# Performance work log

Measured on AMD Instinct MI355X. Metric: run time of the kernel, lower is better.

The kernel has to match this reference:

```python
import jax, jax.numpy as jnp
import numpy as np

N, T, DIN, DH = 100000, 512, 256, 256


def setup_inputs() -> dict:
    key = jax.random.key(0)
    ks = jax.random.split(key, 7)
    s_in = 1.0 / np.sqrt(DH)  # torch GRU init scale
    X = jax.random.normal(ks[0], (N, DIN), dtype=jnp.float32)
    H = (jax.random.uniform(ks[1], (N, T)) < 0.02).astype(jnp.float32)
    W_ih = jax.random.uniform(ks[2], (3 * DH, DIN), minval=-s_in, maxval=s_in, dtype=jnp.float32)
    W_hh = jax.random.uniform(ks[3], (3 * DH, DH), minval=-s_in, maxval=s_in, dtype=jnp.float32)
    b_ih = jax.random.uniform(ks[4], (3 * DH,), minval=-s_in, maxval=s_in, dtype=jnp.float32)
    b_hh = jax.random.uniform(ks[5], (3 * DH,), minval=-s_in, maxval=s_in, dtype=jnp.float32)
    w_att = jax.random.uniform(ks[6], (DH,), minval=-s_in, maxval=s_in, dtype=jnp.float32)
    return {"X": X, "H": H, "W_ih": W_ih, "W_hh": W_hh, "b_ih": b_ih, "b_hh": b_hh, "w_att": w_att}


def _gru(visit_emb, W_ih, W_hh, b_ih, b_hh):
    # torch GRU gate order: r, z, n
    dh = W_hh.shape[1]
    gx = visit_emb @ W_ih.T + b_ih  # [T, 3H] precomputed input projections

    def step(h, gx_t):
        gh = h @ W_hh.T + b_hh  # [3H]
        r = jax.nn.sigmoid(gx_t[:dh] + gh[:dh])
        z = jax.nn.sigmoid(gx_t[dh:2 * dh] + gh[dh:2 * dh])
        n = jnp.tanh(gx_t[2 * dh:] + r * gh[2 * dh:])
        h_new = (1.0 - z) * n + z * h
        return h_new, h_new

    h0 = jnp.zeros((dh,), dtype=visit_emb.dtype)
    _, hs = jax.lax.scan(step, h0, gx)
    return hs  # [T, H]


def reference(X, H, W_ih, W_hh, b_ih, b_hh, w_att):
    visit_emb = H.T @ X  # [T, Din] incidence aggregation
    hidden = _gru(visit_emb, W_ih, W_hh, b_ih, b_hh)  # [T, H]
    alpha = jax.nn.softmax(hidden @ w_att, axis=0)  # [T]
    # diag(alpha) @ hidden summed over T == alpha-weighted sum
    return jnp.einsum("t,th->h", alpha, hidden)
```

## Files before the change

kernel.cpp:

```cpp
#include <hip/hip_runtime.h>
#include <hip/hip_bf16.h>

#define N_ROWS 100000
#define T_DIM  512
#define DIN    256
#define DH     256
#define KC     800
#define NSTEP  25
#define NCHUNK 125

typedef __attribute__((ext_vector_type(8))) short s16x8;
typedef __attribute__((ext_vector_type(4))) float f32x4;
typedef _Float16 h2 __attribute__((ext_vector_type(2)));
typedef _Float16 h8 __attribute__((ext_vector_type(8)));

#if __has_builtin(__builtin_amdgcn_fdot2)
static __device__ __forceinline__ float dot2f(h2 a, h2 b, float c) {
  return __builtin_amdgcn_fdot2(a, b, c, false);
}
#else
static __device__ __forceinline__ float dot2f(h2 a, h2 b, float c) {
  return c + (float)a[0] * (float)b[0] + (float)a[1] * (float)b[1];
}
#endif

static __device__ __forceinline__ unsigned bf16pair(float lo, float hi) {
  unsigned a = __builtin_bit_cast(unsigned, lo);
  unsigned b = __builtin_bit_cast(unsigned, hi);
  a = (a + 0x7fffu + ((a >> 16) & 1u)) >> 16;
  b = (b + 0x7fffu + ((b >> 16) & 1u)) & 0xffff0000u;
  return a | b;
}

__global__ __launch_bounds__(512, 2) void k_agg_mfma(
    const float* __restrict__ X, const float* __restrict__ Hm,
    float* __restrict__ ve, float* __restrict__ ve_part, int use_part)
{
  __shared__ unsigned smem[8192];
  const int tid  = threadIdx.x;
  const int mt   = blockIdx.x & 1;
  const int kc   = blockIdx.x >> 1;
  const int m0   = mt * 256;
  const int k0   = kc * KC;
  const int lane = tid & 63;
  const int wv   = tid >> 6;
  const int wm   = wv >> 2, wn = wv & 3;

  f32x4 acc[8][4] = {};

  const int kp0 = tid >> 6;
  const int kp1 = kp0 + 8;
  const int gg  = tid & 63;

  float4 ra0, ra1, ra2, ra3, rb0, rb1, rb2, rb3;

  auto load_tile = [&](int kt) {
    const size_t kb = (size_t)(k0 + kt * 32);
    const float* pa0 = &Hm[(kb + 2 * kp0) * T_DIM + m0 + gg * 4];
    ra0 = *(const float4*)pa0;
    ra1 = *(const float4*)(pa0 + T_DIM);
    const float* pa1 = &Hm[(kb + 2 * kp1) * T_DIM + m0 + gg * 4];
    ra2 = *(const float4*)pa1;
    ra3 = *(const float4*)(pa1 + T_DIM);
    const float* pb0 = &X[(kb + 2 * kp0) * DIN + gg * 4];
    rb0 = *(const float4*)pb0;
    rb1 = *(const float4*)(pb0 + DIN);
    const float* pb1 = &X[(kb + 2 * kp1) * DIN + gg * 4];
    rb2 = *(const float4*)pb1;
    rb3 = *(const float4*)(pb1 + DIN);
  };

  auto store_tile = [&]() {
#pragma unroll
    for (int d = 0; d < 4; ++d) {
      const int m  = gg * 4 + d;
      const int sw = d << 2;
      smem[m * 16 + (kp0 ^ sw)]        = bf16pair(((const float*)&ra0)[d], ((const float*)&ra1)[d]);
      smem[m * 16 + (kp1 ^ sw)]        = bf16pair(((const float*)&ra2)[d], ((const float*)&ra3)[d]);
      smem[4096 + m * 16 + (kp0 ^ sw)] = bf16pair(((const float*)&rb0)[d], ((const float*)&rb1)[d]);
      smem[4096 + m * 16 + (kp1 ^ sw)] = bf16pair(((const float*)&rb2)[d], ((const float*)&rb3)[d]);
    }
  };

  auto compute = [&]() {
    const uint4* sv = (const uint4*)smem;
    s16x8 af[8], bfr[4];
#pragma unroll
    for (int fm = 0; fm < 8; ++fm) {
      const int m = wm * 128 + fm * 16 + (lane & 15);
      af[fm] = __builtin_bit_cast(s16x8, sv[m * 4 + ((lane >> 4) ^ (m & 3))]);
    }
#pragma unroll
    for (int fn = 0; fn < 4; ++fn) {
      const int n = wn * 64 + fn * 16 + (lane & 15);
      bfr[fn] = __builtin_bit_cast(s16x8, sv[1024 + n * 4 + ((lane >> 4) ^ (n & 3))]);
    }
#pragma unroll
    for (int fm = 0; fm < 8; ++fm)
#pragma unroll
      for (int fn = 0; fn < 4; ++fn)
        acc[fm][fn] = __builtin_amdgcn_mfma_f32_16x16x32_bf16(af[fm], bfr[fn], acc[fm][fn], 0, 0, 0);
  };

  load_tile(0);
  store_tile();
  for (int kt = 0; kt < NSTEP; ++kt) {
    __syncthreads();
    if (kt + 1 < NSTEP) load_tile(kt + 1);
    compute();
    __syncthreads();
    if (kt + 1 < NSTEP) store_tile();
  }

  if (use_part) {
    float* dst = ve_part + (size_t)kc * (512 * 256);
#pragma unroll
    for (int fm = 0; fm < 8; ++fm) {
      const int r0 = m0 + wm * 128 + fm * 16 + (lane >> 4) * 4;
#pragma unroll
      for (int fn = 0; fn < 4; ++fn) {
        const int cc = wn * 64 + fn * 16 + (lane & 15);
#pragma unroll
        for (int q = 0; q < 4; ++q)
          dst[(size_t)(r0 + q) * 256 + cc] = acc[fm][fn][q];
      }
    }
  } else {
#pragma unroll
    for (int fm = 0; fm < 8; ++fm) {
      const int r0 = m0 + wm * 128 + fm * 16 + (lane >> 4) * 4;
#pragma unroll
      for (int fn = 0; fn < 4; ++fn) {
        const int cc = wn * 64 + fn * 16 + (lane & 15);
#pragma unroll
        for (int q = 0; q < 4; ++q)
          atomicAdd(&ve[(size_t)(r0 + q) * 256 + cc], acc[fm][fn][q]);
      }
    }
  }
}

__global__ __launch_bounds__(256) void k_gx(
    const float* __restrict__ vesrc, int npart,
    const float* __restrict__ Wih, const float* __restrict__ bih,
    float* __restrict__ gx)
{
  __shared__ float vl[DIN];
  const int t = blockIdx.x, j = threadIdx.x;
  float s = 0.f;
  for (int p = 0; p < npart; ++p) s += vesrc[(size_t)p * (512 * 256) + t * DIN + j];
  vl[j] = s;
  __syncthreads();
  float a0 = bih[j], a1 = bih[256 + j], a2 = bih[512 + j];
  const float* __restrict__ w0 = &Wih[(size_t)j * DIN];
  const float* __restrict__ w1 = &Wih[(size_t)(j + 256) * DIN];
  const float* __restrict__ w2 = &Wih[(size_t)(j + 512) * DIN];
#pragma unroll 4
  for (int k = 0; k < DIN; ++k) {
    const float v = vl[k];
    a0 = fmaf(w0[k], v, a0);
    a1 = fmaf(w1[k], v, a1);
    a2 = fmaf(w2[k], v, a2);
  }
  gx[t * 768 + j]       = a0;
  gx[t * 768 + 256 + j] = a1;
  gx[t * 768 + 512 + j] = a2;
}

__global__ __launch_bounds__(768, 3) void k_gru_att(
    const float* __restrict__ Whh, const float* __restrict__ bhh,
    const float* __restrict__ gx, const float* __restrict__ watt,
    float* __restrict__ hs, float* __restrict__ out)
{
  __shared__ h8 hbuf8[DH / 8];
  __shared__ float gh[768];
  __shared__ float red[2];
  const int j = threadIdx.x;

  h2 w[128];
  {
    const float2* __restrict__ row = (const float2*)&Whh[(size_t)j * DH];
#pragma unroll
    for (int c = 0; c < 128; ++c) {
      const float2 p = row[c];
      h2 v; v[0] = (_Float16)p.x; v[1] = (_Float16)p.y;
      w[c] = v;
    }
  }
  float bhr = 0.f, bhz = 0.f, bhn = 0.f, h = 0.f;
  if (j < 256) { bhr = bhh[j]; bhz = bhh[256 + j]; bhn = bhh[512 + j]; }
  _Float16* hb = (_Float16*)hbuf8;
  if (j < 256) hb[j] = (_Float16)0.f;
  __syncthreads();

  for (int t = 0; t < T_DIM; ++t) {
    float gxr = 0.f, gxz = 0.f, gxn = 0.f;
    if (j < 256) {
      gxr = gx[t * 768 + j];
      gxz = gx[t * 768 + 256 + j];
      gxn = gx[t * 768 + 512 + j];
    }
    float a0 = 0.f, a1 = 0.f, a2 = 0.f, a3 = 0.f;
#pragma unroll
    for (int c = 0; c < 32; ++c) {
      const h8 hv = hbuf8[c];
      const h2 p0 = __builtin_shufflevector(hv, hv, 0, 1);
      const h2 p1 = __builtin_shufflevector(hv, hv, 2, 3);
      const h2 p2 = __builtin_shufflevector(hv, hv, 4, 5);
      const h2 p3 = __builtin_shufflevector(hv, hv, 6, 7);
      a0 = dot2f(w[4 * c + 0], p0, a0);
      a1 = dot2f(w[4 * c + 1], p1, a1);
      a2 = dot2f(w[4 * c + 2], p2, a2);
      a3 = dot2f(w[4 * c + 3], p3, a3);
    }
    gh[j] = (a0 + a1) + (a2 + a3);
    __syncthreads();
    if (j < 256) {
      const float pr = gxr + gh[j] + bhr;
      const float pz = gxz + gh[256 + j] + bhz;
      const float gn = gh[512 + j] + bhn;
      const float r = 1.f / (1.f + __expf(-pr));
      const float z = 1.f / (1.f + __expf(-pz));
      const float pn = gxn + r * gn;
      const float n = 2.f / (1.f + __expf(-2.f * pn)) - 1.f;
      h = (1.f - z) * n + z * h;
      hs[t * DH + j] = h;
      hb[j] = (_Float16)h;
    }
    __syncthreads();
  }

  if (j < T_DIM) {
    const float* __restrict__ hr = &hs[j * DH];
    float s = 0.f;
#pragma unroll 4
    for (int k = 0; k < DH; ++k) s = fmaf(hr[k], watt[k], s);
    gh[j] = s;
  }
  __syncthreads();
  if (j < 64) {
    float m = -1e30f;
#pragma unroll
    for (int i = 0; i < 8; ++i) m = fmaxf(m, gh[j * 8 + i]);
#pragma unroll
    for (int off = 32; off > 0; off >>= 1) m = fmaxf(m, __shfl_down(m, off));
    if (j == 0) red[0] = m;
  }
  __syncthreads();
  const float M = red[0];
  if (j < T_DIM) gh[j] = __expf(gh[j] - M);
  __syncthreads();
  if (j < 64) {
    float s = 0.f;
#pragma unroll
    for (int i = 0; i < 8; ++i) s += gh[j * 8 + i];
#pragma unroll
    for (int off = 32; off > 0; off >>= 1) s += __shfl_down(s, off);
    if (j == 0) red[1] = s;
  }
  __syncthreads();
  const float inv = 1.f / red[1];
  if (j < 256) {
    float acc = 0.f;
    for (int t = 0; t < T_DIM; ++t) acc = fmaf(gh[t], hs[t * DH + j], acc);
    out[j] = acc * inv;
  }
}

extern "C" void kernel_launch(void* const* d_in, const int* in_sizes, int n_in,
                              void* d_out, int out_size, void* d_ws, size_t ws_size,
                              hipStream_t stream) {
  const float* X    = (const float*)d_in[0];
  const float* H    = (const float*)d_in[1];
  const float* Wih  = (const float*)d_in[2];
  const float* Whh  = (const float*)d_in[3];
  const float* bih  = (const float*)d_in[4];
  const float* bhh  = (const float*)d_in[5];
  const float* watt = (const float*)d_in[6];
  float* out = (float*)d_out;

  char* ws = (char*)d_ws;
  float* gx      = (float*)ws;
  float* hs      = (float*)(ws + 1572864);
  float* ve      = (float*)(ws + 2097152);
  float* ve_part = (float*)(ws + 2621440);

  const size_t need_part = 2621440 + 65536000;
  const int use_part = (ws_size >= need_part) ? 1 : 0;

  if (!use_part)
    hipMemsetAsync(ve, 0, T_DIM * DIN * sizeof(float), stream);

  k_agg_mfma<<<2 * NCHUNK, 512, 0, stream>>>(X, H, ve, ve_part, use_part);
  k_gx<<<T_DIM, 256, 0, stream>>>(use_part ? ve_part : ve, use_part ? NCHUNK : 1,
                                  Wih, bih, gx);
  k_gru_att<<<1, 768, 0, stream>>>(Whh, bhh, gx, watt, hs, out);
}
```

Before: 972.3 us.

## Give each GRU thread all three gate rows to drop shared-memory exchange

Shrinks the recurrent GRU kernel from 768 to 256 threads, with each thread holding its r, z and n weight rows in registers (384 half2 values). Each thread now computes all three gate dot products itself, so the gh shared-memory round trip and one barrier phase per step are gone, and every thread does gate math instead of a third of them sitting idle. In exchange each thread does three times the dot-product work per step, and register pressure is very high, risking spills despite the one-wave-per-EU attribute.

```diff
diff --git a/kernel.cpp b/kernel.cpp
--- a/kernel.cpp
+++ b/kernel.cpp
@@ -167,40 +167,44 @@
   gx[t * 768 + 512 + j] = a2;
 }
 
-__global__ __launch_bounds__(768, 3) void k_gru_att(
+__global__ __launch_bounds__(256, 1) __attribute__((amdgpu_waves_per_eu(1, 1)))
+void k_gru_att(
     const float* __restrict__ Whh, const float* __restrict__ bhh,
     const float* __restrict__ gx, const float* __restrict__ watt,
     float* __restrict__ hs, float* __restrict__ out)
 {
   __shared__ h8 hbuf8[DH / 8];
-  __shared__ float gh[768];
+  __shared__ float sc[T_DIM];
+  __shared__ float wa[DH];
   __shared__ float red[2];
   const int j = threadIdx.x;
 
-  h2 w[128];
+  h2 wr[128], wz[128], wn[128];
   {
-    const float2* __restrict__ row = (const float2*)&Whh[(size_t)j * DH];
+    const float2* __restrict__ pr = (const float2*)&Whh[(size_t)j * DH];
+    const float2* __restrict__ pz = (const float2*)&Whh[(size_t)(j + 256) * DH];
+    const float2* __restrict__ pn = (const float2*)&Whh[(size_t)(j + 512) * DH];
 #pragma unroll
     for (int c = 0; c < 128; ++c) {
-      const float2 p = row[c];
-      h2 v; v[0] = (_Float16)p.x; v[1] = (_Float16)p.y;
-      w[c] = v;
-    }
-  }
-  float bhr = 0.f, bhz = 0.f, bhn = 0.f, h = 0.f;
-  if (j < 256) { bhr = bhh[j]; bhz = bhh[256 + j]; bhn = bhh[512 + j]; }
+      float2 p = pr[c]; h2 v; v[0] = (_Float16)p.x; v[1] = (_Float16)p.y; wr[c] = v;
+      p = pz[c]; v[0] = (_Float16)p.x; v[1] = (_Float16)p.y; wz[c] = v;
+      p = pn[c]; v[0] = (_Float16)p.x; v[1] = (_Float16)p.y; wn[c] = v;
+    }
+  }
+  const float bhr = bhh[j], bhz = bhh[DH + j], bhn = bhh[2 * DH + j];
+  float h = 0.f;
   _Float16* hb = (_Float16*)hbuf8;
-  if (j < 256) hb[j] = (_Float16)0.f;
+  hb[j] = (_Float16)0.f;
+  wa[j] = watt[j];
   __syncthreads();
 
   for (int t = 0; t < T_DIM; ++t) {
-    float gxr = 0.f, gxz = 0.f, gxn = 0.f;
-    if (j < 256) {
-      gxr = gx[t * 768 + j];
-      gxz = gx[t * 768 + 256 + j];
-      gxn = gx[t * 768 + 512 + j];
-    }
-    float a0 = 0.f, a1 = 0.f, a2 = 0.f, a3 = 0.f;
+    const float gxr = gx[t * 768 + j];
+    const float gxz = gx[t * 768 + DH + j];
+    const float gxn = gx[t * 768 + 2 * DH + j];
+    float ra0 = 0.f, ra1 = 0.f, ra2 = 0.f, ra3 = 0.f;
+    float za0 = 0.f, za1 = 0.f, za2 = 0.f, za3 = 0.f;
+    float na0 = 0.f, na1 = 0.f, na2 = 0.f, na3 = 0.f;
 #pragma unroll
     for (int c = 0; c < 32; ++c) {
       const h8 hv = hbuf8[c];
@@ -208,63 +212,69 @@
       const h2 p1 = __builtin_shufflevector(hv, hv, 2, 3);
       const h2 p2 = __builtin_shufflevector(hv, hv, 4, 5);
       const h2 p3 = __builtin_shufflevector(hv, hv, 6, 7);
-      a0 = dot2f(w[4 * c + 0], p0, a0);
-      a1 = dot2f(w[4 * c + 1], p1, a1);
-      a2 = dot2f(w[4 * c + 2], p2, a2);
-      a3 = dot2f(w[4 * c + 3], p3, a3);
-    }
-    gh[j] = (a0 + a1) + (a2 + a3);
+      ra0 = dot2f(wr[4 * c + 0], p0, ra0);
+      ra1 = dot2f(wr[4 * c + 1], p1, ra1);
+      ra2 = dot2f(wr[4 * c + 2], p2, ra2);
+      ra3 = dot2f(wr[4 * c + 3], p3, ra3);
+      za0 = dot2f(wz[4 * c + 0], p0, za0);
+      za1 = dot2f(wz[4 * c + 1], p1, za1);
+      za2 = dot2f(wz[4 * c + 2], p2, za2);
+      za3 = dot2f(wz[4 * c + 3], p3, za3);
+      na0 = dot2f(wn[4 * c + 0], p0, na0);
+      na1 = dot2f(wn[4 * c + 1], p1, na1);
+      na2 = dot2f(wn[4 * c + 2], p2, na2);
+      na3 = dot2f(wn[4 * c + 3], p3, na3);
+    }
+    const float ghr = (ra0 + ra1) + (ra2 + ra3);
+    const float ghz = (za0 + za1) + (za2 + za3);
+    const float ghn = (na0 + na1) + (na2 + na3);
+    const float r = 1.f / (1.f + __expf(-(gxr + ghr + bhr)));
+    const float z = 1.f / (1.f + __expf(-(gxz + ghz + bhz)));
+    const float pn = gxn + r * (ghn + bhn);
+    const float n = 2.f / (1.f + __expf(-2.f * pn)) - 1.f;
+    h = (1.f - z) * n + z * h;
+    hs[t * DH + j] = h;
     __syncthreads();
-    if (j < 256) {
-      const float pr = gxr + gh[j] + bhr;
-      const float pz = gxz + gh[256 + j] + bhz;
-      const float gn = gh[512 + j] + bhn;
-      const float r = 1.f / (1.f + __expf(-pr));
-      const float z = 1.f / (1.f + __expf(-pz));
-      const float pn = gxn + r * gn;
-      const float n = 2.f / (1.f + __expf(-2.f * pn)) - 1.f;
-      h = (1.f - z) * n + z * h;
-      hs[t * DH + j] = h;
-      hb[j] = (_Float16)h;
-    }
+    hb[j] = (_Float16)h;
     __syncthreads();
   }
 
-  if (j < T_DIM) {
-    const float* __restrict__ hr = &hs[j * DH];
+#pragma unroll
+  for (int tt = 0; tt < 2; ++tt) {
+    const int t = j + tt * 256;
+    const float* __restrict__ hr = &hs[t * DH];
     float s = 0.f;
 #pragma unroll 4
-    for (int k = 0; k < DH; ++k) s = fmaf(hr[k], watt[k], s);
-    gh[j] = s;
+    for (int k = 0; k < DH; ++k) s = fmaf(hr[k], wa[k], s);
+    sc[t] = s;
   }
   __syncthreads();
   if (j < 64) {
     float m = -1e30f;
 #pragma unroll
-    for (int i = 0; i < 8; ++i) m = fmaxf(m, gh[j * 8 + i]);
+    for (int i = 0; i < 8; ++i) m = fmaxf(m, sc[j * 8 + i]);
 #pragma unroll
     for (int off = 32; off > 0; off >>= 1) m = fmaxf(m, __shfl_down(m, off));
     if (j == 0) red[0] = m;
   }
   __syncthreads();
   const float M = red[0];
-  if (j < T_DIM) gh[j] = __expf(gh[j] - M);
+#pragma unroll
+  for (int tt = 0; tt < 2; ++tt) sc[j + tt * 256] = __expf(sc[j + tt * 256] - M);
   __syncthreads();
   if (j < 64) {
     float s = 0.f;
 #pragma unroll
-    for (int i = 0; i < 8; ++i) s += gh[j * 8 + i];
+    for (int i = 0; i < 8; ++i) s += sc[j * 8 + i];
 #pragma unroll
     for (int off = 32; off > 0; off >>= 1) s += __shfl_down(s, off);
     if (j == 0) red[1] = s;
   }
   __syncthreads();
   const float inv = 1.f / red[1];
-  if (j < 256) {
-    float acc = 0.f;
-    for (int t = 0; t < T_DIM; ++t) acc = fmaf(gh[t], hs[t * DH + j], acc);
-    out[j] = acc * inv;
-  }
+  float acc = 0.f;
+  for (int t = 0; t < T_DIM; ++t) acc = fmaf(sc[t], hs[t * DH + j], acc);
+  out[j] = acc * inv;
 }
 
 extern "C" void kernel_launch(void* const* d_in, const int* in_sizes, int n_in,
@@ -294,5 +304,5 @@
   k_agg_mfma<<<2 * NCHUNK, 512, 0, stream>>>(X, H, ve, ve_part, use_part);
   k_gx<<<T_DIM, 256, 0, stream>>>(use_part ? ve_part : ve, use_part ? NCHUNK : 1,
                                   Wih, bih, gx);
-  k_gru_att<<<1, 768, 0, stream>>>(Whh, bhh, gx, watt, hs, out);
-}
+  k_gru_att<<<1, 256, 0, stream>>>(Whh, bhh, gx, watt, hs, out);
+}
```

After: 1.627 ms. +67.3%, slower.

## Compute GRU recurrent matvec with bf16 MFMA instead of per-thread fp16 dot2

Applied to the files above, without the earlier changes.

The serial GRU kernel now keeps W_hh as bf16 MFMA A-fragments in registers across 8 waves of 512 threads. Each timestep runs 16x16x32 MFMAs against the broadcast hidden state, replacing 768 threads that each did 128 fdot2 operations. The hh bias is folded into the accumulator init. The final attention pooling is split across two halves of the block and uses vectorized loads. This targets the latency of the 512-step recurrence, and bf16 weights and hidden state carry less mantissa precision than the previous fp16.

```diff
diff --git a/kernel.cpp b/kernel.cpp
--- a/kernel.cpp
+++ b/kernel.cpp
@@ -11,18 +11,6 @@
 
 typedef __attribute__((ext_vector_type(8))) short s16x8;
 typedef __attribute__((ext_vector_type(4))) float f32x4;
-typedef _Float16 h2 __attribute__((ext_vector_type(2)));
-typedef _Float16 h8 __attribute__((ext_vector_type(8)));
-
-#if __has_builtin(__builtin_amdgcn_fdot2)
-static __device__ __forceinline__ float dot2f(h2 a, h2 b, float c) {
-  return __builtin_amdgcn_fdot2(a, b, c, false);
-}
-#else
-static __device__ __forceinline__ float dot2f(h2 a, h2 b, float c) {
-  return c + (float)a[0] * (float)b[0] + (float)a[1] * (float)b[1];
-}
-#endif
 
 static __device__ __forceinline__ unsigned bf16pair(float lo, float hi) {
   unsigned a = __builtin_bit_cast(unsigned, lo);
@@ -167,104 +155,133 @@
   gx[t * 768 + 512 + j] = a2;
 }
 
-__global__ __launch_bounds__(768, 3) void k_gru_att(
+__global__ __launch_bounds__(512, 2) void k_gru_att(
     const float* __restrict__ Whh, const float* __restrict__ bhh,
     const float* __restrict__ gx, const float* __restrict__ watt,
     float* __restrict__ hs, float* __restrict__ out)
 {
-  __shared__ h8 hbuf8[DH / 8];
-  __shared__ float gh[768];
+  __shared__ __hip_bfloat16 hb[DH];
+  __shared__ float ghs[768];
+  __shared__ float bsh[768];
+  __shared__ float sc[T_DIM];
   __shared__ float red[2];
-  const int j = threadIdx.x;
-
-  h2 w[128];
-  {
-    const float2* __restrict__ row = (const float2*)&Whh[(size_t)j * DH];
-#pragma unroll
-    for (int c = 0; c < 128; ++c) {
-      const float2 p = row[c];
-      h2 v; v[0] = (_Float16)p.x; v[1] = (_Float16)p.y;
-      w[c] = v;
-    }
-  }
-  float bhr = 0.f, bhz = 0.f, bhn = 0.f, h = 0.f;
-  if (j < 256) { bhr = bhh[j]; bhz = bhh[256 + j]; bhn = bhh[512 + j]; }
-  _Float16* hb = (_Float16*)hbuf8;
-  if (j < 256) hb[j] = (_Float16)0.f;
+
+  const int tid = threadIdx.x;
+  const int w   = tid >> 6;
+  const int l   = tid & 63;
+  const int lr  = l & 15;
+  const int lg  = l >> 4;
+
+  int rowbase[6];
+  rowbase[0] = w * 32;       rowbase[1] = w * 32 + 16;
+  rowbase[2] = 256 + w * 32; rowbase[3] = 256 + w * 32 + 16;
+  rowbase[4] = 512 + w * 32; rowbase[5] = 512 + w * 32 + 16;
+
+  s16x8 wf[6][8];
+#pragma unroll
+  for (int tt = 0; tt < 6; ++tt) {
+    const float* rp = &Whh[(size_t)(rowbase[tt] + lr) * DH + lg * 8];
+#pragma unroll
+    for (int kb = 0; kb < 8; ++kb) {
+      const float4 x0 = *(const float4*)(rp + kb * 32);
+      const float4 x1 = *(const float4*)(rp + kb * 32 + 4);
+      uint4 uu;
+      uu.x = bf16pair(x0.x, x0.y);
+      uu.y = bf16pair(x0.z, x0.w);
+      uu.z = bf16pair(x1.x, x1.y);
+      uu.w = bf16pair(x1.z, x1.w);
+      wf[tt][kb] = __builtin_bit_cast(s16x8, uu);
+    }
+  }
+
+  bsh[tid] = bhh[tid < 768 ? tid : 0];
+  if (tid < 256) {
+    bsh[512 + tid] = bhh[512 + tid];
+    hb[tid] = __float2bfloat16(0.0f);
+  }
+  float h = 0.f;
   __syncthreads();
 
   for (int t = 0; t < T_DIM; ++t) {
     float gxr = 0.f, gxz = 0.f, gxn = 0.f;
-    if (j < 256) {
-      gxr = gx[t * 768 + j];
-      gxz = gx[t * 768 + 256 + j];
-      gxn = gx[t * 768 + 512 + j];
-    }
-    float a0 = 0.f, a1 = 0.f, a2 = 0.f, a3 = 0.f;
-#pragma unroll
-    for (int c = 0; c < 32; ++c) {
-      const h8 hv = hbuf8[c];
-      const h2 p0 = __builtin_shufflevector(hv, hv, 0, 1);
-      const h2 p1 = __builtin_shufflevector(hv, hv, 2, 3);
-      const h2 p2 = __builtin_shufflevector(hv, hv, 4, 5);
-      const h2 p3 = __builtin_shufflevector(hv, hv, 6, 7);
-      a0 = dot2f(w[4 * c + 0], p0, a0);
-      a1 = dot2f(w[4 * c + 1], p1, a1);
-      a2 = dot2f(w[4 * c + 2], p2, a2);
-      a3 = dot2f(w[4 * c + 3], p3, a3);
-    }
-    gh[j] = (a0 + a1) + (a2 + a3);
+    if (tid < 256) {
+      gxr = gx[t * 768 + tid];
+      gxz = gx[t * 768 + 256 + tid];
+      gxn = gx[t * 768 + 512 + tid];
+    }
+    f32x4 acc[6];
+#pragma unroll
+    for (int tt = 0; tt < 6; ++tt)
+      acc[tt] = *(const f32x4*)&bsh[rowbase[tt] + lg * 4];
+#pragma unroll
+    for (int kb = 0; kb < 8; ++kb) {
+      const s16x8 bf = *(const s16x8*)((const char*)hb + kb * 64 + lg * 16);
+#pragma unroll
+      for (int tt = 0; tt < 6; ++tt)
+        acc[tt] = __builtin_amdgcn_mfma_f32_16x16x32_bf16(wf[tt][kb], bf, acc[tt], 0, 0, 0);
+    }
+    if (lr == 0) {
+#pragma unroll
+      for (int tt = 0; tt < 6; ++tt)
+        *(f32x4*)&ghs[rowbase[tt] + lg * 4] = acc[tt];
+    }
     __syncthreads();
-    if (j < 256) {
-      const float pr = gxr + gh[j] + bhr;
-      const float pz = gxz + gh[256 + j] + bhz;
-      const float gn = gh[512 + j] + bhn;
-      const float r = 1.f / (1.f + __expf(-pr));
-      const float z = 1.f / (1.f + __expf(-pz));
-      const float pn = gxn + r * gn;
+    if (tid < 256) {
+      const float r = 1.f / (1.f + __expf(-(gxr + ghs[tid])));
+      const float z = 1.f / (1.f + __expf(-(gxz + ghs[256 + tid])));
+      const float pn = gxn + r * ghs[512 + tid];
       const float n = 2.f / (1.f + __expf(-2.f * pn)) - 1.f;
       h = (1.f - z) * n + z * h;
-      hs[t * DH + j] = h;
-      hb[j] = (_Float16)h;
+      hs[t * DH + tid] = h;
+      hb[tid] = __float2bfloat16(h);
     }
     __syncthreads();
   }
 
-  if (j < T_DIM) {
-    const float* __restrict__ hr = &hs[j * DH];
+  {
+    const float* __restrict__ hr = &hs[tid * DH];
     float s = 0.f;
 #pragma unroll 4
-    for (int k = 0; k < DH; ++k) s = fmaf(hr[k], watt[k], s);
-    gh[j] = s;
-  }
-  __syncthreads();
-  if (j < 64) {
+    for (int k = 0; k < DH; k += 4) {
+      const float4 hv = *(const float4*)(hr + k);
+      const float4 wv4 = *(const float4*)(watt + k);
+      s = fmaf(hv.x, wv4.x, s); s = fmaf(hv.y, wv4.y, s);
+      s = fmaf(hv.z, wv4.z, s); s = fmaf(hv.w, wv4.w, s);
+    }
+    sc[tid] = s;
+  }
+  __syncthreads();
+  if (tid < 64) {
     float m = -1e30f;
 #pragma unroll
-    for (int i = 0; i < 8; ++i) m = fmaxf(m, gh[j * 8 + i]);
+    for (int i = 0; i < 8; ++i) m = fmaxf(m, sc[tid * 8 + i]);
 #pragma unroll
     for (int off = 32; off > 0; off >>= 1) m = fmaxf(m, __shfl_down(m, off));
-    if (j == 0) red[0] = m;
+    if (tid == 0) red[0] = m;
   }
   __syncthreads();
   const float M = red[0];
-  if (j < T_DIM) gh[j] = __expf(gh[j] - M);
-  __syncthreads();
-  if (j < 64) {
+  sc[tid] = __expf(sc[tid] - M);
+  __syncthreads();
+  if (tid < 64) {
     float s = 0.f;
 #pragma unroll
-    for (int i = 0; i < 8; ++i) s += gh[j * 8 + i];
+    for (int i = 0; i < 8; ++i) s += sc[tid * 8 + i];
 #pragma unroll
     for (int off = 32; off > 0; off >>= 1) s += __shfl_down(s, off);
-    if (j == 0) red[1] = s;
+    if (tid == 0) red[1] = s;
   }
   __syncthreads();
   const float inv = 1.f / red[1];
-  if (j < 256) {
+  {
+    const int j = tid & 255, half = tid >> 8;
     float acc = 0.f;
-    for (int t = 0; t < T_DIM; ++t) acc = fmaf(gh[t], hs[t * DH + j], acc);
-    out[j] = acc * inv;
-  }
+    for (int t = half * 256; t < half * 256 + 256; ++t)
+      acc = fmaf(sc[t], hs[t * DH + j], acc);
+    bsh[half * 256 + j] = acc;
+  }
+  __syncthreads();
+  if (tid < 256) out[tid] = (bsh[tid] + bsh[256 + tid]) * inv;
 }
 
 extern "C" void kernel_launch(void* const* d_in, const int* in_sizes, int n_in,
@@ -294,5 +311,5 @@
   k_agg_mfma<<<2 * NCHUNK, 512, 0, stream>>>(X, H, ve, ve_part, use_part);
   k_gx<<<T_DIM, 256, 0, stream>>>(use_part ? ve_part : ve, use_part ? NCHUNK : 1,
                                   Wih, bih, gx);
-  k_gru_att<<<1, 768, 0, stream>>>(Whh, bhh, gx, watt, hs, out);
-}
+  k_gru_att<<<1, 512, 0, stream>>>(Whh, bhh, gx, watt, hs, out);
+}
```

Result: slower. 1.030 ms (+5.9%).
